# Optimization experiments

Measured on AMD Instinct MI355X. Metric: run time of the kernel, lower is better.

## Reference

```python
import jax, jax.numpy as jnp
import numpy as np
import itertools

D_FEAT = 8      # feature dim per point
N_NBR = 16     # kNN neighbors (self.N)
ORDERS = (2, 3)
BIG = 99999999.0


def _to_select(N, order):
    # rows: [0] + each (order-1)-combination of {1..N-1}, first N-1 rows
    rows = [[0] + list(c) for c in itertools.combinations(range(1, N), order - 1)][:N - 1]
    return np.asarray(rows, dtype=np.int32)  # (N-1, order)


def setup_inputs() -> dict:
    key = jax.random.key(0)
    ks = jax.random.split(key, 18)
    B, NP, DM, DO, NM, PNM = 4, 4096, 16, 8, 64, 64
    r = lambda k, s: jax.random.normal(k, s, dtype=jnp.float32)
    return {
        "x": r(ks[0], (B, NP * D_FEAT)),
        "z": r(ks[1], (B, PNM)),
        "Wm2": r(ks[2], (2, DM)) * 0.5, "bm2": r(ks[3], (DM,)) * 0.1,
        "Wm3": r(ks[4], (3, DM)) * 0.5, "bm3": r(ks[5], (DM,)) * 0.1,
        "Wv2": r(ks[6], (2, DM)) * 0.5, "bv2": r(ks[7], (DM,)) * 0.1,
        "Wv3": r(ks[8], (3, DM)) * 0.5, "bv3": r(ks[9], (DM,)) * 0.1,
        "Wmx": r(ks[10], (2 * DM, DO)) * 0.1, "bmx": r(ks[11], (DO,)) * 0.1,
        "Wvx": r(ks[12], (2 * DM, NM)) * 0.1, "bvx": r(ks[13], (NM,)) * 0.1,
        "Wmz": r(ks[14], (PNM, DO)) * 0.1, "bmz": r(ks[15], (DO,)) * 0.1,
        "Wvz": r(ks[16], (PNM, NM)) * 0.1, "bvz": r(ks[17], (NM,)) * 0.1,
    }


def _forward(x, z, Wm2, bm2, Wm3, bm3, Wv2, bv2, Wv3, bv3,
             Wmx, bmx, Wvx, bvx, Wmz, bmz, Wvz, bvz):
    B = x.shape[0]
    NP = x.shape[1] // D_FEAT
    N = N_NBR
    x3 = x.reshape(B, NP, D_FEAT)

    # pairwise euclidean distances via gram trick (avoids B*NP*NP*D intermediate)
    n2 = jnp.sum(x3 * x3, axis=-1)                                   # (B, NP)
    d2 = n2[:, :, None] + n2[:, None, :] - 2.0 * jnp.einsum('bid,bjd->bij', x3, x3)
    dist = jnp.sqrt(jnp.maximum(d2, 0.0))                            # (B, NP, NP)
    dist = jnp.where(dist == 0.0, BIG, dist)                         # mask exact-zero distances
    diag = jnp.arange(NP)
    dist = dist.at[:, diag, diag].set(BIG)                           # self-distance (exactly 0 in torch)

    # N smallest, sorted ascending
    _, idx = jax.lax.top_k(-dist, N)                                 # idx: (B, NP, N)

    def order_feats(Wf, bf, order):
        ts = jnp.asarray(_to_select(N, order))                       # (N-1, order)
        sel = idx[:, :, ts]                                          # (B, NP, N-1, o)
        g = jax.vmap(lambda xb, sb: xb[sb])(x3, sel)                 # (B, NP, N-1, o, D)
        # Linear(order -> d_Mfeat) applied per feature-dim o-tuple, relu, mean over feature dims
        y = jax.nn.relu(jnp.einsum('bnrod,ok->bnrdk', g, Wf) + bf)   # (B, NP, N-1, D, K)
        return y.mean(axis=3).reshape(B, NP * (N - 1), -1)           # (B, NP*(N-1), K)

    moments = jnp.concatenate([order_feats(Wm2, bm2, 2), order_feats(Wm3, bm3, 3)], axis=-1)
    v_moments = jnp.concatenate([order_feats(Wv2, bv2, 2), order_feats(Wv3, bv3, 3)], axis=-1)

    d_out = Wmx.shape[1]
    x_new = jax.nn.relu(moments @ Wmx + bmx + (z @ Wmz + bmz)[:, None, :])
    x_new = x_new.reshape(B, NP, N - 1, d_out).mean(axis=2).reshape(B, NP * d_out)

    z_new = jax.nn.relu(v_moments @ Wvx + bvx + (z @ Wvz + bvz)[:, None, :]).mean(axis=1)
    return x_new, z_new


def reference(x, z, Wm2, bm2, Wm3, bm3, Wv2, bv2, Wv3, bv3,
              Wmx, bmx, Wvx, bvx, Wmz, bmz, Wvz, bvz):
    return _forward(x, z, Wm2, bm2, Wm3, bm3, Wv2, bv2, Wv3, bv3,
                    Wmx, bmx, Wvx, bvx, Wmz, bmz, Wvz, bvz)
```

## Files before the change

### kernel.cpp

```cpp
#include <hip/hip_runtime.h>
#include <hip/hip_bf16.h>

#define BIGF 99999999.0f
#define NPP 4096
#define BB 4
#define NQ 4
#define CAP 128

typedef float f32x2 __attribute__((ext_vector_type(2)));

__device__ __forceinline__ f32x2 pk_fma(f32x2 a, f32x2 b, f32x2 c) {
    f32x2 d;
    asm("v_pk_fma_f32 %0, %1, %2, %3" : "=v"(d) : "v"(a), "v"(b), "v"(c));
    return d;
}


template <typename T>
__device__ __forceinline__ T bitonic_sort64(T v, int lane) {
    #pragma unroll
    for (int k = 2; k <= 64; k <<= 1) {
        #pragma unroll
        for (int j = k >> 1; j > 0; j >>= 1) {
            T p = __shfl_xor(v, j);
            bool up  = ((lane & k) == 0);
            bool low = ((lane & j) == 0);
            T mn = (v < p) ? v : p;
            T mx = (v < p) ? p : v;
            v = (up == low) ? mn : mx;
        }
    }
    return v;
}

__device__ __forceinline__ float dot8_pk(const f32x2* qp, f32x2 p0, f32x2 p1,
                                         f32x2 p2, f32x2 p3) {
    f32x2 acc = {0.f, 0.f};
    acc = pk_fma(qp[0], p0, acc);
    acc = pk_fma(qp[1], p1, acc);
    acc = pk_fma(qp[2], p2, acc);
    acc = pk_fma(qp[3], p3, acc);
    return acc.x + acc.y;
}


__global__ __launch_bounds__(256) void n2_kernel(
    const float* __restrict__ x, const float* __restrict__ z,
    const float* __restrict__ Wmz, const float* __restrict__ bmz,
    const float* __restrict__ Wvz, const float* __restrict__ bvz,
    float* __restrict__ n2tab, float* __restrict__ zzm, float* __restrict__ zzv,
    float* __restrict__ zout)
{
    int i = blockIdx.x * 256 + threadIdx.x;
    const float4* p = (const float4*)(x + (long)i * 8);
    float4 a = p[0], c = p[1];
    float s = 0.f;
    s = fmaf(a.x, a.x, s); s = fmaf(a.y, a.y, s);
    s = fmaf(a.z, a.z, s); s = fmaf(a.w, a.w, s);
    s = fmaf(c.x, c.x, s); s = fmaf(c.y, c.y, s);
    s = fmaf(c.z, c.z, s); s = fmaf(c.w, c.w, s);
    n2tab[i] = s;

    if (blockIdx.x == 0) {
        zout[threadIdx.x] = 0.f;
        int b = threadIdx.x >> 6, l = threadIdx.x & 63;
        float sv = 0.f;
        for (int q = 0; q < 64; ++q) sv = fmaf(z[b * 64 + q], Wvz[q * 64 + l], sv);
        zzv[b * 64 + l] = sv + bvz[l];
        if (threadIdx.x < 32) {
            int bm = threadIdx.x >> 3, lm = threadIdx.x & 7;
            float sm = 0.f;
            for (int q = 0; q < 64; ++q) sm = fmaf(z[bm * 64 + q], Wmz[q * 8 + lm], sm);
            zzm[bm * 8 + lm] = sm + bmz[lm];
        }
    }
}


__global__ __launch_bounds__(256) void knn_kernel(const float* __restrict__ x,
                                                  const float* __restrict__ n2tab,
                                                  int* __restrict__ idx_out) {
    __shared__ unsigned long long cand[4][NQ][CAP];
    __shared__ unsigned cnt_s[4][NQ];

    int lane = threadIdx.x & 63;
    int wid  = threadIdx.x >> 6;
    if (lane < NQ) cnt_s[wid][lane] = 0;

    int gw   = blockIdx.x * 4 + wid;
    int q0   = gw * NQ;
    int b    = q0 >> 12;
    int qloc = q0 & 4095;
    const float* xb = x + (long)b * NPP * 8;
    const float* nb = n2tab + b * NPP;

    f32x2 qp[NQ][4];
    float n2i[NQ];
    int selfT[NQ], selfL[NQ];
    #pragma unroll
    for (int q = 0; q < NQ; ++q) {
        const f32x2* qsrc = (const f32x2*)(xb + (long)(qloc + q) * 8);
        #pragma unroll
        for (int e = 0; e < 4; ++e) qp[q][e] = qsrc[e];
        n2i[q]   = nb[qloc + q];
        selfT[q] = (qloc + q) >> 6;
        selfL[q] = (qloc + q) & 63;
    }
    const unsigned BIGB = __float_as_uint(BIGF);

    unsigned minb[NQ];
    #pragma unroll
    for (int q = 0; q < NQ; ++q) minb[q] = 0xFFFFFFFFu;

    #pragma unroll 4
    for (int t = 0; t < 64; ++t) {
        int j = t * 64 + lane;
        const f32x2* pj = (const f32x2*)(xb + (long)j * 8);
        f32x2 p0 = pj[0], p1 = pj[1], p2 = pj[2], p3 = pj[3];
        float n2j = nb[j];
        #pragma unroll
        for (int q = 0; q < NQ; ++q) {
            float dot = dot8_pk(qp[q], p0, p1, p2, p3);
            float d2  = fmaf(-2.0f, dot, n2i[q] + n2j);
            unsigned kb = (d2 <= 0.0f) ? BIGB : __float_as_uint(d2);
            if (t == selfT[q]) {
                kb = (lane == selfL[q]) ? BIGB : kb;
            }
            minb[q] = (kb < minb[q]) ? kb : minb[q];
        }
    }

    unsigned T[NQ];
    #pragma unroll
    for (int q = 0; q < NQ; ++q) {
        unsigned s = bitonic_sort64(minb[q], lane);
        T[q] = (unsigned)__shfl((int)s, 15);
    }

    #pragma unroll 4
    for (int t = 0; t < 64; ++t) {
        int j = t * 64 + lane;
        const f32x2* pj = (const f32x2*)(xb + (long)j * 8);
        f32x2 p0 = pj[0], p1 = pj[1], p2 = pj[2], p3 = pj[3];
        float n2j = nb[j];
        unsigned kb[NQ];
        bool hit = false;
        #pragma unroll
        for (int q = 0; q < NQ; ++q) {
            float dot = dot8_pk(qp[q], p0, p1, p2, p3);
            float d2  = fmaf(-2.0f, dot, n2i[q] + n2j);
            unsigned k = (d2 <= 0.0f) ? BIGB : __float_as_uint(d2);
            if (t == selfT[q]) {
                k = (lane == selfL[q]) ? BIGB : k;
            }
            kb[q] = k;
            hit |= (k <= T[q]);
        }
        if (__any(hit)) {
            #pragma unroll
            for (int q = 0; q < NQ; ++q) {
                if (kb[q] <= T[q]) {
                    unsigned old = atomicAdd(&cnt_s[wid][q], 1u);
                    if (old < CAP) {
                        cand[wid][q][old] =
                            ((unsigned long long)kb[q] << 32) | (unsigned)j;
                    }
                }
            }
        }
    }

    #pragma unroll 1
    for (int q = 0; q < NQ; ++q) {
        unsigned nc = cnt_s[wid][q];
        int n = nc > CAP ? CAP : (int)nc;
        unsigned long long v = (lane < n) ? cand[wid][q][lane] : ~0ull;
        unsigned long long R = bitonic_sort64(v, lane);
        if (n > 64) {
            unsigned long long w2 = (64 + lane < n) ? cand[wid][q][64 + lane] : ~0ull;
            w2 = bitonic_sort64(w2, lane);
            unsigned long long vt = __shfl(w2, lane - 16);
            unsigned long long comb = (lane < 16) ? R : ((lane < 32) ? vt : ~0ull);
            R = bitonic_sort64(comb, lane);
        }
        if (lane < 16) {
            idx_out[(long)(q0 + q) * 16 + lane] = (int)(R & 0xFFFFFFFFull);
        }
    }
}


__global__ __launch_bounds__(256) void feat_kernel(
    const float* __restrict__ x, const int* __restrict__ idxw,
    const float* __restrict__ Wm2, const float* __restrict__ bm2,
    const float* __restrict__ Wm3, const float* __restrict__ bm3,
    const float* __restrict__ Wv2, const float* __restrict__ bv2,
    const float* __restrict__ Wv3, const float* __restrict__ bv3,
    const float* __restrict__ Wmx, const float* __restrict__ bmx,
    const float* __restrict__ Wvx, const float* __restrict__ bvx,
    const float* __restrict__ zzm, const float* __restrict__ zzv,
    float* __restrict__ xout, float* __restrict__ zout)
{
    int lane = threadIdx.x & 63;
    int wid  = threadIdx.x >> 6;
    int pn   = blockIdx.x * 4 + wid;
    int b    = pn >> 12;
    const float* xb = x + b * NPP * 8;

    __shared__ float xg_s[4][16][8];
    __shared__ float mo_s[4][15][68];
    __shared__ float wmxT_s[8][36];
    __shared__ float bzm_s[8];
    __shared__ float zpart[4][64];

    if (threadIdx.x < 256) {
        wmxT_s[threadIdx.x & 7][threadIdx.x >> 3] = Wmx[threadIdx.x];
    }
    if (threadIdx.x < 8) bzm_s[threadIdx.x] = bmx[threadIdx.x] + zzm[b * 8 + threadIdx.x];

    int k = lane & 15;
    float w20 = Wm2[k], w21 = Wm2[16 + k], bb2 = bm2[k];
    float w30 = Wm3[k], w31 = Wm3[16 + k], w32 = Wm3[32 + k], bb3 = bm3[k];
    float u20 = Wv2[k], u21 = Wv2[16 + k], cc2 = bv2[k];
    float u30 = Wv3[k], u31 = Wv3[16 + k], u32 = Wv3[32 + k], cc3 = bv3[k];

    int g  = lane >> 5;
    int nm = lane & 31;
    float wvxa[32], wvxb[32];
    #pragma unroll
    for (int c = 0; c < 32; ++c) {
        wvxa[c] = Wvx[c * 64 + nm];
        wvxb[c] = Wvx[c * 64 + nm + 32];
    }
    float bz3a = bvx[nm]      + zzv[b * 64 + nm];
    float bz3b = bvx[nm + 32] + zzv[b * 64 + nm + 32];

    if (lane < 16) {
        int myid = idxw[(long)pn * 16 + lane];
        const float4* ps = (const float4*)(xb + (long)myid * 8);
        float4 a = ps[0], c4 = ps[1];
        *((float4*)&xg_s[wid][lane][0]) = a;
        *((float4*)&xg_s[wid][lane][4]) = c4;
    }
    __syncthreads();

    float4 g0l = *(const float4*)&xg_s[wid][0][0];
    float4 g0h = *(const float4*)&xg_s[wid][0][4];
    float g0[8] = {g0l.x, g0l.y, g0l.z, g0l.w, g0h.x, g0h.y, g0h.z, g0h.w};

    #pragma unroll
    for (int p = 0; p < 4; ++p) {
        int rg = lane >> 4;
        int r  = p * 4 + rg;
        int rc = (r < 14) ? r : 14;
        int i2  = rc + 1;
        int i3a = (rc < 14) ? 1 : 2;
        int i3b = (rc < 14) ? rc + 2 : 3;
        float4 a1 = *(const float4*)&xg_s[wid][i2][0];
        float4 b1 = *(const float4*)&xg_s[wid][i2][4];
        float4 aa = *(const float4*)&xg_s[wid][i3a][0];
        float4 ba = *(const float4*)&xg_s[wid][i3a][4];
        float4 ab = *(const float4*)&xg_s[wid][i3b][0];
        float4 bb = *(const float4*)&xg_s[wid][i3b][4];
        float G1[8]  = {a1.x, a1.y, a1.z, a1.w, b1.x, b1.y, b1.z, b1.w};
        float G3a[8] = {aa.x, aa.y, aa.z, aa.w, ba.x, ba.y, ba.z, ba.w};
        float G3b[8] = {ab.x, ab.y, ab.z, ab.w, bb.x, bb.y, bb.z, bb.w};
        float s2 = 0.f, s3 = 0.f, t2 = 0.f, t3 = 0.f;
        #pragma unroll
        for (int d = 0; d < 8; ++d) {
            float gz = g0[d], g1 = G1[d], ga = G3a[d], gb = G3b[d];
            float y2 = fmaf(gz, w20, fmaf(g1, w21, bb2));
            s2 += fmaxf(y2, 0.f);
            float y3 = fmaf(gz, w30, fmaf(ga, w31, fmaf(gb, w32, bb3)));
            s3 += fmaxf(y3, 0.f);
            float z2 = fmaf(gz, u20, fmaf(g1, u21, cc2));
            t2 += fmaxf(z2, 0.f);
            float z3 = fmaf(gz, u30, fmaf(ga, u31, fmaf(gb, u32, cc3)));
            t3 += fmaxf(z3, 0.f);
        }
        if (r < 15) {
            mo_s[wid][r][k]      = s2 * 0.125f;
            mo_s[wid][r][16 + k] = s3 * 0.125f;
            mo_s[wid][r][32 + k] = t2 * 0.125f;
            mo_s[wid][r][48 + k] = t3 * 0.125f;
        }
    }
    __syncthreads();

    float xa = 0.f;
    #pragma unroll
    for (int half = 0; half < 2; ++half) {
        int r   = (lane >> 3) + half * 8;
        int doo = lane & 7;
        float s = 0.f;
        if (r < 15) {
            s = bzm_s[doo];
            #pragma unroll
            for (int cc = 0; cc < 8; ++cc) {
                float4 v = *(const float4*)&mo_s[wid][r][cc * 4];
                float4 w = *(const float4*)&wmxT_s[doo][cc * 4];
                s = fmaf(v.x, w.x, s);
                s = fmaf(v.y, w.y, s);
                s = fmaf(v.z, w.z, s);
                s = fmaf(v.w, w.w, s);
            }
            s = fmaxf(s, 0.f);
        }
        xa += s;
    }
    xa += __shfl_xor(xa, 8);
    xa += __shfl_xor(xa, 16);
    xa += __shfl_xor(xa, 32);
    float xv = xa * (1.0f / 15.0f);
    if (lane < 8) xout[(long)pn * 8 + lane] = xv;

    float A = 0.f, Bz = 0.f;
    #pragma unroll 1
    for (int rr = 0; rr < 8; ++rr) {
        int r = g * 8 + rr;
        if (r < 15) {
            const float* row = &mo_s[wid][r][32];
            float sa = bz3a, sb = bz3b;
            #pragma unroll
            for (int cc = 0; cc < 8; ++cc) {
                float4 v = *(const float4*)(row + cc * 4);
                sa = fmaf(v.x, wvxa[cc * 4 + 0], sa);
                sb = fmaf(v.x, wvxb[cc * 4 + 0], sb);
                sa = fmaf(v.y, wvxa[cc * 4 + 1], sa);
                sb = fmaf(v.y, wvxb[cc * 4 + 1], sb);
                sa = fmaf(v.z, wvxa[cc * 4 + 2], sa);
                sb = fmaf(v.z, wvxb[cc * 4 + 2], sb);
                sa = fmaf(v.w, wvxa[cc * 4 + 3], sa);
                sb = fmaf(v.w, wvxb[cc * 4 + 3], sb);
            }
            A  += fmaxf(sa, 0.f);
            Bz += fmaxf(sb, 0.f);
        }
    }
    A  += __shfl_xor(A, 32);
    Bz += __shfl_xor(Bz, 32);
    float za = ((g == 0) ? A : Bz) * (1.0f / 61440.0f);
    zpart[wid][lane] = za;
    __syncthreads();
    if (wid == 0) {
        float ssum = zpart[0][lane] + zpart[1][lane] + zpart[2][lane] + zpart[3][lane];
        atomicAdd(&zout[b * 64 + lane], ssum);
    }
}


extern "C" void kernel_launch(void* const* d_in, const int* in_sizes, int n_in,
                              void* d_out, int out_size, void* d_ws, size_t ws_size,
                              hipStream_t stream) {
    const float* x   = (const float*)d_in[0];
    const float* z   = (const float*)d_in[1];
    const float* Wm2 = (const float*)d_in[2];
    const float* bm2 = (const float*)d_in[3];
    const float* Wm3 = (const float*)d_in[4];
    const float* bm3 = (const float*)d_in[5];
    const float* Wv2 = (const float*)d_in[6];
    const float* bv2 = (const float*)d_in[7];
    const float* Wv3 = (const float*)d_in[8];
    const float* bv3 = (const float*)d_in[9];
    const float* Wmx = (const float*)d_in[10];
    const float* bmx = (const float*)d_in[11];
    const float* Wvx = (const float*)d_in[12];
    const float* bvx = (const float*)d_in[13];
    const float* Wmz = (const float*)d_in[14];
    const float* bmz = (const float*)d_in[15];
    const float* Wvz = (const float*)d_in[16];
    const float* bvz = (const float*)d_in[17];

    float* out  = (float*)d_out;
    int*   idxw = (int*)d_ws;
    float* zzm  = (float*)((char*)d_ws + (size_t)BB * NPP * 16 * 4);
    float* zzv  = zzm + BB * 8;
    float* n2t  = zzv + BB * 64;
    float* xout = out;
    float* zout = out + BB * NPP * 8;

    n2_kernel<<<dim3(BB * NPP / 256), dim3(256), 0, stream>>>(
        x, z, Wmz, bmz, Wvz, bvz, n2t, zzm, zzv, zout);
    knn_kernel<<<dim3(BB * NPP / (4 * NQ)), dim3(256), 0, stream>>>(x, n2t, idxw);
    feat_kernel<<<dim3(4096), dim3(256), 0, stream>>>(
        x, idxw, Wm2, bm2, Wm3, bm3, Wv2, bv2, Wv3, bv3,
        Wmx, bmx, Wvx, bvx, zzm, zzv, xout, zout);
}
```

Before: 241.1 us.

## Fuse kNN selection and feature MLP into a single kernel

Merges the kNN kernel and the feature kernel, so each wave writes its 16 neighbor indices to shared memory and immediately gathers and processes the features of its 4 query points. This removes the global index round-trip and one kernel launch. The threshold pre-pass now scans only every other tile, which loosens the candidate threshold and raises the risk of more candidates than CAP. The zero-distance masking is dropped. The Wmx and Wvx products now use packed FMAs, and the candidate and moment buffers share one shared-memory region.

```diff
diff --git a/kernel.cpp b/kernel.cpp
--- a/kernel.cpp
+++ b/kernel.cpp
@@ -1,20 +1,19 @@
 #include <hip/hip_runtime.h>
 #include <hip/hip_bf16.h>
 
-#define BIGF 99999999.0f
 #define NPP 4096
 #define BB 4
 #define NQ 4
 #define CAP 128
 
 typedef float f32x2 __attribute__((ext_vector_type(2)));
+typedef unsigned long long u64;
 
 __device__ __forceinline__ f32x2 pk_fma(f32x2 a, f32x2 b, f32x2 c) {
     f32x2 d;
     asm("v_pk_fma_f32 %0, %1, %2, %3" : "=v"(d) : "v"(a), "v"(b), "v"(c));
     return d;
 }
-
 
 template <typename T>
 __device__ __forceinline__ T bitonic_sort64(T v, int lane) {
@@ -77,121 +76,8 @@
 }
 
 
-__global__ __launch_bounds__(256) void knn_kernel(const float* __restrict__ x,
-                                                  const float* __restrict__ n2tab,
-                                                  int* __restrict__ idx_out) {
-    __shared__ unsigned long long cand[4][NQ][CAP];
-    __shared__ unsigned cnt_s[4][NQ];
-
-    int lane = threadIdx.x & 63;
-    int wid  = threadIdx.x >> 6;
-    if (lane < NQ) cnt_s[wid][lane] = 0;
-
-    int gw   = blockIdx.x * 4 + wid;
-    int q0   = gw * NQ;
-    int b    = q0 >> 12;
-    int qloc = q0 & 4095;
-    const float* xb = x + (long)b * NPP * 8;
-    const float* nb = n2tab + b * NPP;
-
-    f32x2 qp[NQ][4];
-    float n2i[NQ];
-    int selfT[NQ], selfL[NQ];
-    #pragma unroll
-    for (int q = 0; q < NQ; ++q) {
-        const f32x2* qsrc = (const f32x2*)(xb + (long)(qloc + q) * 8);
-        #pragma unroll
-        for (int e = 0; e < 4; ++e) qp[q][e] = qsrc[e];
-        n2i[q]   = nb[qloc + q];
-        selfT[q] = (qloc + q) >> 6;
-        selfL[q] = (qloc + q) & 63;
-    }
-    const unsigned BIGB = __float_as_uint(BIGF);
-
-    unsigned minb[NQ];
-    #pragma unroll
-    for (int q = 0; q < NQ; ++q) minb[q] = 0xFFFFFFFFu;
-
-    #pragma unroll 4
-    for (int t = 0; t < 64; ++t) {
-        int j = t * 64 + lane;
-        const f32x2* pj = (const f32x2*)(xb + (long)j * 8);
-        f32x2 p0 = pj[0], p1 = pj[1], p2 = pj[2], p3 = pj[3];
-        float n2j = nb[j];
-        #pragma unroll
-        for (int q = 0; q < NQ; ++q) {
-            float dot = dot8_pk(qp[q], p0, p1, p2, p3);
-            float d2  = fmaf(-2.0f, dot, n2i[q] + n2j);
-            unsigned kb = (d2 <= 0.0f) ? BIGB : __float_as_uint(d2);
-            if (t == selfT[q]) {
-                kb = (lane == selfL[q]) ? BIGB : kb;
-            }
-            minb[q] = (kb < minb[q]) ? kb : minb[q];
-        }
-    }
-
-    unsigned T[NQ];
-    #pragma unroll
-    for (int q = 0; q < NQ; ++q) {
-        unsigned s = bitonic_sort64(minb[q], lane);
-        T[q] = (unsigned)__shfl((int)s, 15);
-    }
-
-    #pragma unroll 4
-    for (int t = 0; t < 64; ++t) {
-        int j = t * 64 + lane;
-        const f32x2* pj = (const f32x2*)(xb + (long)j * 8);
-        f32x2 p0 = pj[0], p1 = pj[1], p2 = pj[2], p3 = pj[3];
-        float n2j = nb[j];
-        unsigned kb[NQ];
-        bool hit = false;
-        #pragma unroll
-        for (int q = 0; q < NQ; ++q) {
-            float dot = dot8_pk(qp[q], p0, p1, p2, p3);
-            float d2  = fmaf(-2.0f, dot, n2i[q] + n2j);
-            unsigned k = (d2 <= 0.0f) ? BIGB : __float_as_uint(d2);
-            if (t == selfT[q]) {
-                k = (lane == selfL[q]) ? BIGB : k;
-            }
-            kb[q] = k;
-            hit |= (k <= T[q]);
-        }
-        if (__any(hit)) {
-            #pragma unroll
-            for (int q = 0; q < NQ; ++q) {
-                if (kb[q] <= T[q]) {
-                    unsigned old = atomicAdd(&cnt_s[wid][q], 1u);
-                    if (old < CAP) {
-                        cand[wid][q][old] =
-                            ((unsigned long long)kb[q] << 32) | (unsigned)j;
-                    }
-                }
-            }
-        }
-    }
-
-    #pragma unroll 1
-    for (int q = 0; q < NQ; ++q) {
-        unsigned nc = cnt_s[wid][q];
-        int n = nc > CAP ? CAP : (int)nc;
-        unsigned long long v = (lane < n) ? cand[wid][q][lane] : ~0ull;
-        unsigned long long R = bitonic_sort64(v, lane);
-        if (n > 64) {
-            unsigned long long w2 = (64 + lane < n) ? cand[wid][q][64 + lane] : ~0ull;
-            w2 = bitonic_sort64(w2, lane);
-            unsigned long long vt = __shfl(w2, lane - 16);
-            unsigned long long comb = (lane < 16) ? R : ((lane < 32) ? vt : ~0ull);
-            R = bitonic_sort64(comb, lane);
-        }
-        if (lane < 16) {
-            idx_out[(long)(q0 + q) * 16 + lane] = (int)(R & 0xFFFFFFFFull);
-        }
-    }
-}
-
-
-__global__ __launch_bounds__(256) void feat_kernel(
-    const float* __restrict__ x, const int* __restrict__ idxw,
+__global__ __launch_bounds__(256) void fused_kernel(
+    const float* __restrict__ x, const float* __restrict__ n2tab,
     const float* __restrict__ Wm2, const float* __restrict__ bm2,
     const float* __restrict__ Wm3, const float* __restrict__ bm3,
     const float* __restrict__ Wv2, const float* __restrict__ bv2,
@@ -201,22 +87,115 @@
     const float* __restrict__ zzm, const float* __restrict__ zzv,
     float* __restrict__ xout, float* __restrict__ zout)
 {
+    __shared__ __align__(16) char ubuf[4][4352];
+    __shared__ float xg_s[4][NQ][16][8];
+    __shared__ int   idx_s[4][NQ][16];
+    __shared__ float wmxT_s[8][40];
+    __shared__ float bzm_s[8];
+    __shared__ float zpart[4][64];
+    __shared__ unsigned cnt_s[4][NQ];
+
     int lane = threadIdx.x & 63;
     int wid  = threadIdx.x >> 6;
-    int pn   = blockIdx.x * 4 + wid;
-    int b    = pn >> 12;
-    const float* xb = x + b * NPP * 8;
-
-    __shared__ float xg_s[4][16][8];
-    __shared__ float mo_s[4][15][68];
-    __shared__ float wmxT_s[8][36];
-    __shared__ float bzm_s[8];
-    __shared__ float zpart[4][64];
-
-    if (threadIdx.x < 256) {
-        wmxT_s[threadIdx.x & 7][threadIdx.x >> 3] = Wmx[threadIdx.x];
-    }
-    if (threadIdx.x < 8) bzm_s[threadIdx.x] = bmx[threadIdx.x] + zzm[b * 8 + threadIdx.x];
+    int gw   = blockIdx.x * 4 + wid;
+    int q0   = gw * NQ;
+    int b    = q0 >> 12;
+    int qloc = q0 & 4095;
+    const float* xb = x + (long)b * NPP * 8;
+    const float* nb = n2tab + b * NPP;
+
+    if (threadIdx.x < 256) wmxT_s[threadIdx.x & 7][threadIdx.x >> 3] = Wmx[threadIdx.x];
+    if (threadIdx.x < 8)   bzm_s[threadIdx.x] = bmx[threadIdx.x] + zzm[b * 8 + threadIdx.x];
+    if (lane < NQ) cnt_s[wid][lane] = 0;
+    __syncthreads();
+
+    f32x2 qp[NQ][4];
+    float n2i[NQ];
+    int selfT[NQ], selfL[NQ];
+    #pragma unroll
+    for (int q = 0; q < NQ; ++q) {
+        const f32x2* qsrc = (const f32x2*)(xb + (long)(qloc + q) * 8);
+        #pragma unroll
+        for (int e = 0; e < 4; ++e) qp[q][e] = qsrc[e];
+        n2i[q]   = nb[qloc + q];
+        selfT[q] = (qloc + q) >> 6;
+        selfL[q] = (qloc + q) & 63;
+    }
+
+    unsigned minb[NQ];
+    #pragma unroll
+    for (int q = 0; q < NQ; ++q) minb[q] = 0xFFFFFFFFu;
+
+    #pragma unroll 4
+    for (int tt = 0; tt < 32; ++tt) {
+        int t = tt * 2;
+        int j = t * 64 + lane;
+        const f32x2* pj = (const f32x2*)(xb + (long)j * 8);
+        f32x2 p0 = pj[0], p1 = pj[1], p2 = pj[2], p3 = pj[3];
+        float n2j = nb[j];
+        #pragma unroll
+        for (int q = 0; q < NQ; ++q) {
+            float dot = dot8_pk(qp[q], p0, p1, p2, p3);
+            float d2  = fmaf(-2.0f, dot, n2i[q] + n2j);
+            unsigned kb = __float_as_uint(d2);
+            if (t == selfT[q]) kb = (lane == selfL[q]) ? 0xFFFFFFFFu : kb;
+            minb[q] = (kb < minb[q]) ? kb : minb[q];
+        }
+    }
+
+    unsigned T[NQ];
+    #pragma unroll
+    for (int q = 0; q < NQ; ++q) {
+        unsigned s = bitonic_sort64(minb[q], lane);
+        T[q] = (unsigned)__shfl((int)s, 15);
+    }
+
+    u64* cand = (u64*)ubuf[wid];
+    #pragma unroll 2
+    for (int t = 0; t < 64; ++t) {
+        int j = t * 64 + lane;
+        const f32x2* pj = (const f32x2*)(xb + (long)j * 8);
+        f32x2 p0 = pj[0], p1 = pj[1], p2 = pj[2], p3 = pj[3];
+        float n2j = nb[j];
+        #pragma unroll
+        for (int q = 0; q < NQ; ++q) {
+            float dot = dot8_pk(qp[q], p0, p1, p2, p3);
+            float d2  = fmaf(-2.0f, dot, n2i[q] + n2j);
+            unsigned kb = __float_as_uint(d2);
+            if (t == selfT[q]) kb = (lane == selfL[q]) ? 0xFFFFFFFFu : kb;
+            if (kb <= T[q]) {
+                unsigned old = atomicAdd(&cnt_s[wid][q], 1u);
+                if (old < CAP) cand[q * CAP + old] = ((u64)kb << 32) | (unsigned)j;
+            }
+        }
+    }
+
+    #pragma unroll 1
+    for (int q = 0; q < NQ; ++q) {
+        unsigned nc = cnt_s[wid][q];
+        int n = nc > CAP ? CAP : (int)nc;
+        u64 v = (lane < n) ? cand[q * CAP + lane] : ~0ull;
+        u64 R = bitonic_sort64(v, lane);
+        if (n > 64) {
+            u64 w2 = (64 + lane < n) ? cand[q * CAP + 64 + lane] : ~0ull;
+            w2 = bitonic_sort64(w2, lane);
+            u64 vt = __shfl(w2, lane - 16);
+            u64 comb = (lane < 16) ? R : ((lane < 32) ? vt : ~0ull);
+            R = bitonic_sort64(comb, lane);
+        }
+        if (lane < 16) idx_s[wid][q][lane] = (int)(R & 0xFFFFFFFFull);
+    }
+
+    #pragma unroll
+    for (int p = 0; p < NQ; ++p) {
+        if (lane < 16) {
+            int id = idx_s[wid][p][lane];
+            const float4* ps = (const float4*)(xb + (long)id * 8);
+            float4 A = ps[0], C = ps[1];
+            *((float4*)&xg_s[wid][p][lane][0]) = A;
+            *((float4*)&xg_s[wid][p][lane][4]) = C;
+        }
+    }
 
     int k = lane & 15;
     float w20 = Wm2[k], w21 = Wm2[16 + k], bb2 = bm2[k];
@@ -226,120 +205,107 @@
 
     int g  = lane >> 5;
     int nm = lane & 31;
-    float wvxa[32], wvxb[32];
-    #pragma unroll
-    for (int c = 0; c < 32; ++c) {
-        wvxa[c] = Wvx[c * 64 + nm];
-        wvxb[c] = Wvx[c * 64 + nm + 32];
+    f32x2 wa2[16], wb2[16];
+    #pragma unroll
+    for (int cc = 0; cc < 16; ++cc) {
+        wa2[cc].x = Wvx[(2 * cc) * 64 + nm];
+        wa2[cc].y = Wvx[(2 * cc + 1) * 64 + nm];
+        wb2[cc].x = Wvx[(2 * cc) * 64 + nm + 32];
+        wb2[cc].y = Wvx[(2 * cc + 1) * 64 + nm + 32];
     }
     float bz3a = bvx[nm]      + zzv[b * 64 + nm];
     float bz3b = bvx[nm + 32] + zzv[b * 64 + nm + 32];
 
-    if (lane < 16) {
-        int myid = idxw[(long)pn * 16 + lane];
-        const float4* ps = (const float4*)(xb + (long)myid * 8);
-        float4 a = ps[0], c4 = ps[1];
-        *((float4*)&xg_s[wid][lane][0]) = a;
-        *((float4*)&xg_s[wid][lane][4]) = c4;
-    }
-    __syncthreads();
-
-    float4 g0l = *(const float4*)&xg_s[wid][0][0];
-    float4 g0h = *(const float4*)&xg_s[wid][0][4];
-    float g0[8] = {g0l.x, g0l.y, g0l.z, g0l.w, g0h.x, g0h.y, g0h.z, g0h.w};
-
-    #pragma unroll
-    for (int p = 0; p < 4; ++p) {
-        int rg = lane >> 4;
-        int r  = p * 4 + rg;
-        int rc = (r < 14) ? r : 14;
-        int i2  = rc + 1;
-        int i3a = (rc < 14) ? 1 : 2;
-        int i3b = (rc < 14) ? rc + 2 : 3;
-        float4 a1 = *(const float4*)&xg_s[wid][i2][0];
-        float4 b1 = *(const float4*)&xg_s[wid][i2][4];
-        float4 aa = *(const float4*)&xg_s[wid][i3a][0];
-        float4 ba = *(const float4*)&xg_s[wid][i3a][4];
-        float4 ab = *(const float4*)&xg_s[wid][i3b][0];
-        float4 bb = *(const float4*)&xg_s[wid][i3b][4];
-        float G1[8]  = {a1.x, a1.y, a1.z, a1.w, b1.x, b1.y, b1.z, b1.w};
-        float G3a[8] = {aa.x, aa.y, aa.z, aa.w, ba.x, ba.y, ba.z, ba.w};
-        float G3b[8] = {ab.x, ab.y, ab.z, ab.w, bb.x, bb.y, bb.z, bb.w};
-        float s2 = 0.f, s3 = 0.f, t2 = 0.f, t3 = 0.f;
-        #pragma unroll
-        for (int d = 0; d < 8; ++d) {
-            float gz = g0[d], g1 = G1[d], ga = G3a[d], gb = G3b[d];
-            float y2 = fmaf(gz, w20, fmaf(g1, w21, bb2));
-            s2 += fmaxf(y2, 0.f);
-            float y3 = fmaf(gz, w30, fmaf(ga, w31, fmaf(gb, w32, bb3)));
-            s3 += fmaxf(y3, 0.f);
-            float z2 = fmaf(gz, u20, fmaf(g1, u21, cc2));
-            t2 += fmaxf(z2, 0.f);
-            float z3 = fmaf(gz, u30, fmaf(ga, u31, fmaf(gb, u32, cc3)));
-            t3 += fmaxf(z3, 0.f);
-        }
-        if (r < 15) {
-            mo_s[wid][r][k]      = s2 * 0.125f;
-            mo_s[wid][r][16 + k] = s3 * 0.125f;
-            mo_s[wid][r][32 + k] = t2 * 0.125f;
-            mo_s[wid][r][48 + k] = t3 * 0.125f;
-        }
-    }
-    __syncthreads();
-
-    float xa = 0.f;
-    #pragma unroll
-    for (int half = 0; half < 2; ++half) {
-        int r   = (lane >> 3) + half * 8;
-        int doo = lane & 7;
-        float s = 0.f;
-        if (r < 15) {
-            s = bzm_s[doo];
+    float* mo = (float*)ubuf[wid];
+    float Aacc = 0.f, Bacc = 0.f;
+
+    #pragma unroll 1
+    for (int p = 0; p < NQ; ++p) {
+        float4 g0l = *(const float4*)&xg_s[wid][p][0][0];
+        float4 g0h = *(const float4*)&xg_s[wid][p][0][4];
+        float g0[8] = {g0l.x, g0l.y, g0l.z, g0l.w, g0h.x, g0h.y, g0h.z, g0h.w};
+
+        #pragma unroll
+        for (int pp = 0; pp < 4; ++pp) {
+            int rg = lane >> 4;
+            int r  = pp * 4 + rg;
+            int rc = (r < 14) ? r : 14;
+            int i2  = rc + 1;
+            int i3a = (rc < 14) ? 1 : 2;
+            int i3b = (rc < 14) ? rc + 2 : 3;
+            float4 a1 = *(const float4*)&xg_s[wid][p][i2][0];
+            float4 b1 = *(const float4*)&xg_s[wid][p][i2][4];
+            float4 aa = *(const float4*)&xg_s[wid][p][i3a][0];
+            float4 ba = *(const float4*)&xg_s[wid][p][i3a][4];
+            float4 ab = *(const float4*)&xg_s[wid][p][i3b][0];
+            float4 bb = *(const float4*)&xg_s[wid][p][i3b][4];
+            float G1[8]  = {a1.x, a1.y, a1.z, a1.w, b1.x, b1.y, b1.z, b1.w};
+            float G3a[8] = {aa.x, aa.y, aa.z, aa.w, ba.x, ba.y, ba.z, ba.w};
+            float G3b[8] = {ab.x, ab.y, ab.z, ab.w, bb.x, bb.y, bb.z, bb.w};
+            float s2 = 0.f, s3 = 0.f, t2 = 0.f, t3 = 0.f;
             #pragma unroll
-            for (int cc = 0; cc < 8; ++cc) {
-                float4 v = *(const float4*)&mo_s[wid][r][cc * 4];
-                float4 w = *(const float4*)&wmxT_s[doo][cc * 4];
-                s = fmaf(v.x, w.x, s);
-                s = fmaf(v.y, w.y, s);
-                s = fmaf(v.z, w.z, s);
-                s = fmaf(v.w, w.w, s);
-            }
-            s = fmaxf(s, 0.f);
-        }
-        xa += s;
-    }
-    xa += __shfl_xor(xa, 8);
-    xa += __shfl_xor(xa, 16);
-    xa += __shfl_xor(xa, 32);
-    float xv = xa * (1.0f / 15.0f);
-    if (lane < 8) xout[(long)pn * 8 + lane] = xv;
-
-    float A = 0.f, Bz = 0.f;
-    #pragma unroll 1
-    for (int rr = 0; rr < 8; ++rr) {
-        int r = g * 8 + rr;
-        if (r < 15) {
-            const float* row = &mo_s[wid][r][32];
-            float sa = bz3a, sb = bz3b;
-            #pragma unroll
-            for (int cc = 0; cc < 8; ++cc) {
-                float4 v = *(const float4*)(row + cc * 4);
-                sa = fmaf(v.x, wvxa[cc * 4 + 0], sa);
-                sb = fmaf(v.x, wvxb[cc * 4 + 0], sb);
-                sa = fmaf(v.y, wvxa[cc * 4 + 1], sa);
-                sb = fmaf(v.y, wvxb[cc * 4 + 1], sb);
-                sa = fmaf(v.z, wvxa[cc * 4 + 2], sa);
-                sb = fmaf(v.z, wvxb[cc * 4 + 2], sb);
-                sa = fmaf(v.w, wvxa[cc * 4 + 3], sa);
-                sb = fmaf(v.w, wvxb[cc * 4 + 3], sb);
-            }
-            A  += fmaxf(sa, 0.f);
-            Bz += fmaxf(sb, 0.f);
-        }
-    }
-    A  += __shfl_xor(A, 32);
-    Bz += __shfl_xor(Bz, 32);
-    float za = ((g == 0) ? A : Bz) * (1.0f / 61440.0f);
+            for (int d = 0; d < 8; ++d) {
+                float gz = g0[d], g1 = G1[d], ga = G3a[d], gb = G3b[d];
+                float y2 = fmaf(gz, w20, fmaf(g1, w21, bb2));
+                s2 += fmaxf(y2, 0.f);
+                float y3 = fmaf(gz, w30, fmaf(ga, w31, fmaf(gb, w32, bb3)));
+                s3 += fmaxf(y3, 0.f);
+                float z2 = fmaf(gz, u20, fmaf(g1, u21, cc2));
+                t2 += fmaxf(z2, 0.f);
+                float z3 = fmaf(gz, u30, fmaf(ga, u31, fmaf(gb, u32, cc3)));
+                t3 += fmaxf(z3, 0.f);
+            }
+            if (r < 15) {
+                mo[r * 72 + k]      = s2 * 0.125f;
+                mo[r * 72 + 16 + k] = s3 * 0.125f;
+                mo[r * 72 + 32 + k] = t2 * 0.125f;
+                mo[r * 72 + 48 + k] = t3 * 0.125f;
+            }
+        }
+
+        float xa = 0.f;
+        #pragma unroll
+        for (int half = 0; half < 2; ++half) {
+            int r   = (lane >> 3) + half * 8;
+            int doo = lane & 7;
+            if (r < 15) {
+                const f32x2* vp = (const f32x2*)&mo[r * 72];
+                const f32x2* wp = (const f32x2*)&wmxT_s[doo][0];
+                f32x2 acc = {0.f, 0.f};
+                #pragma unroll
+                for (int cc = 0; cc < 16; ++cc) acc = pk_fma(vp[cc], wp[cc], acc);
+                float s = bzm_s[doo] + acc.x + acc.y;
+                xa += fmaxf(s, 0.f);
+            }
+        }
+        xa += __shfl_xor(xa, 8);
+        xa += __shfl_xor(xa, 16);
+        xa += __shfl_xor(xa, 32);
+        if (lane < 8) xout[(long)(q0 + p) * 8 + lane] = xa * (1.0f / 15.0f);
+
+        #pragma unroll 1
+        for (int rr = 0; rr < 8; ++rr) {
+            int r = g * 8 + rr;
+            if (r < 15) {
+                const f32x2* vp = (const f32x2*)&mo[r * 72 + 32];
+                f32x2 accA = {0.f, 0.f}, accB = {0.f, 0.f};
+                #pragma unroll
+                for (int cc = 0; cc < 16; ++cc) {
+                    f32x2 v = vp[cc];
+                    accA = pk_fma(v, wa2[cc], accA);
+                    accB = pk_fma(v, wb2[cc], accB);
+                }
+                float sa = bz3a + accA.x + accA.y;
+                float sb = bz3b + accB.x + accB.y;
+                Aacc += fmaxf(sa, 0.f);
+                Bacc += fmaxf(sb, 0.f);
+            }
+        }
+    }
+
+    Aacc += __shfl_xor(Aacc, 32);
+    Bacc += __shfl_xor(Bacc, 32);
+    float za = ((g == 0) ? Aacc : Bacc) * (1.0f / 61440.0f);
     zpart[wid][lane] = za;
     __syncthreads();
     if (wid == 0) {
@@ -372,17 +338,15 @@
     const float* bvz = (const float*)d_in[17];
 
     float* out  = (float*)d_out;
-    int*   idxw = (int*)d_ws;
-    float* zzm  = (float*)((char*)d_ws + (size_t)BB * NPP * 16 * 4);
-    float* zzv  = zzm + BB * 8;
-    float* n2t  = zzv + BB * 64;
+    float* zzm  = (float*)d_ws;
+    float* zzv  = zzm + 32;
+    float* n2t  = zzv + 256;
     float* xout = out;
     float* zout = out + BB * NPP * 8;
 
     n2_kernel<<<dim3(BB * NPP / 256), dim3(256), 0, stream>>>(
         x, z, Wmz, bmz, Wvz, bvz, n2t, zzm, zzv, zout);
-    knn_kernel<<<dim3(BB * NPP / (4 * NQ)), dim3(256), 0, stream>>>(x, n2t, idxw);
-    feat_kernel<<<dim3(4096), dim3(256), 0, stream>>>(
-        x, idxw, Wm2, bm2, Wm3, bm3, Wv2, bv2, Wv3, bv3,
+    fused_kernel<<<dim3(BB * NPP / (4 * NQ)), dim3(256), 0, stream>>>(
+        x, n2t, Wm2, bm2, Wm3, bm3, Wv2, bv2, Wv3, bv3,
         Wmx, bmx, Wvx, bvx, zzm, zzv, xout, zout);
 }
```

Result: faster. 217.6 us (-9.7%).
